# Kernel optimization log

Measured on AMD Instinct MI355X. Metric: run time of the kernel, lower is better.

Reference implementation:

```python
import jax, jax.numpy as jnp
import numpy as np

N, K, W = 500000, 512, 64


def setup_inputs() -> dict:
    key = jax.random.key(0)
    kx, kc = jax.random.split(key)
    X = jax.random.normal(kx, (N, W), dtype=jnp.float32)
    # nn.init.uniform_(codebook.weight, a=-1.0, b=1.0)
    codebook = jax.random.uniform(kc, (K, W), dtype=jnp.float32, minval=-1.0, maxval=1.0)
    return {"X": X, "codebook": codebook}


def reference(X, codebook):
    # torch.cdist (p=2): pairwise Euclidean distances [N, K]
    x2 = jnp.sum(X * X, axis=-1, keepdims=True)          # [N, 1]
    c2 = jnp.sum(codebook * codebook, axis=-1)           # [K]
    d2 = x2 - 2.0 * (X @ codebook.T) + c2[None, :]        # [N, K]
    dist = jnp.sqrt(jnp.maximum(d2, 0.0))
    idx = jnp.argmin(dist, axis=-1)                       # [N] int
    min_dists = jnp.min(dist, axis=-1)                    # [N] == gather(dist, idx)
    return idx, min_dists
```

## Files before the change

kernel.cpp:

```cpp
#include <hip/hip_runtime.h>

#define N_POINTS 500000
#define K_CENT   512
#define W_DIM    64
#define N_JOBS   ((N_POINTS + 63) / 64)
#define SCALE_LO 2048.0f
#define INV_LO   (1.0f / 2048.0f)

typedef _Float16 half8 __attribute__((ext_vector_type(8)));
typedef float    f32x16 __attribute__((ext_vector_type(16)));

__global__ void cvt_kernel(const float* __restrict__ cb,
                           _Float16* __restrict__ cbf) {
    int id = blockIdx.x * 256 + threadIdx.x;
    if (id >= K_CENT * 8) return;
    int c = id >> 3, o = (id & 7) * 8;
    int t = c >> 5, r = c & 31;
    int s = o >> 4, half = (o >> 3) & 1;
    int lane = half * 32 + r;
    const float* src = cb + (size_t)c * W_DIM + o;
    half8 h, l;
#pragma unroll
    for (int j = 0; j < 8; ++j) {
        float w = -2.0f * src[j];
        _Float16 hh = (_Float16)w;
        h[j] = hh;
        l[j] = (_Float16)((w - (float)hh) * SCALE_LO);
    }
    size_t base_h = ((size_t)(t * 2 + 0) * 4 + s) * 512 + (size_t)lane * 8;
    size_t base_l = ((size_t)(t * 2 + 1) * 4 + s) * 512 + (size_t)lane * 8;
    *(half8*)(cbf + base_h) = h;
    *(half8*)(cbf + base_l) = l;
}

__global__ void c2_kernel(const float* __restrict__ cb, float* __restrict__ c2) {
    int c = blockIdx.x * 256 + threadIdx.x;
    if (c >= K_CENT) return;
    const float4* row = (const float4*)(cb + (size_t)c * W_DIM);
    double s = 0.0;
#pragma unroll
    for (int j = 0; j < W_DIM / 4; ++j) {
        float4 v = row[j];
        s += (double)v.x * v.x + (double)v.y * v.y + (double)v.z * v.z + (double)v.w * v.w;
    }
    c2[c] = (float)s;
}

#define CHUNK_BODY(T, CURH, CURL, NXTH, NXTL)                                      \
    {                                                                              \
        int t_ = (T);                                                              \
        if (t_ < 15) {                                                             \
            const _Float16* nb = cbf + (size_t)(t_ + 1) * 4096 + (size_t)lane * 8; \
            NXTH[0] = *(const half8*)(nb + 0 * 512);                               \
            NXTH[1] = *(const half8*)(nb + 1 * 512);                               \
            NXTH[2] = *(const half8*)(nb + 2 * 512);                               \
            NXTH[3] = *(const half8*)(nb + 3 * 512);                               \
            NXTL[0] = *(const half8*)(nb + 2048 + 0 * 512);                        \
            NXTL[1] = *(const half8*)(nb + 2048 + 1 * 512);                        \
            NXTL[2] = *(const half8*)(nb + 2048 + 2 * 512);                        \
            NXTL[3] = *(const half8*)(nb + 2048 + 3 * 512);                        \
        }                                                                          \
        float4 q0 = *(const float4*)&c2s[t_ * 32 + half * 4 + 0];                  \
        float4 q1 = *(const float4*)&c2s[t_ * 32 + half * 4 + 8];                  \
        float4 q2 = *(const float4*)&c2s[t_ * 32 + half * 4 + 16];                 \
        float4 q3 = *(const float4*)&c2s[t_ * 32 + half * 4 + 24];                 \
        f32x16 am0, am1, ac0, ac1;                                                 \
        am0[0]=q0.x; am0[1]=q0.y; am0[2]=q0.z; am0[3]=q0.w;                        \
        am0[4]=q1.x; am0[5]=q1.y; am0[6]=q1.z; am0[7]=q1.w;                        \
        am0[8]=q2.x; am0[9]=q2.y; am0[10]=q2.z; am0[11]=q2.w;                      \
        am0[12]=q3.x; am0[13]=q3.y; am0[14]=q3.z; am0[15]=q3.w;                    \
        am1 = am0;                                                                 \
        _Pragma("unroll")                                                          \
        for (int j = 0; j < 16; ++j) { ac0[j] = 0.f; ac1[j] = 0.f; }               \
        _Pragma("unroll")                                                          \
        for (int s = 0; s < 4; ++s) {                                              \
            am0 = __builtin_amdgcn_mfma_f32_32x32x16_f16(CURH[s], b0h[s], am0, 0, 0, 0); \
            am1 = __builtin_amdgcn_mfma_f32_32x32x16_f16(CURH[s], b1h[s], am1, 0, 0, 0); \
            ac0 = __builtin_amdgcn_mfma_f32_32x32x16_f16(CURL[s], b0h[s], ac0, 0, 0, 0); \
            ac1 = __builtin_amdgcn_mfma_f32_32x32x16_f16(CURL[s], b1h[s], ac1, 0, 0, 0); \
            ac0 = __builtin_amdgcn_mfma_f32_32x32x16_f16(CURH[s], b0l[s], ac0, 0, 0, 0); \
            ac1 = __builtin_amdgcn_mfma_f32_32x32x16_f16(CURH[s], b1l[s], ac1, 0, 0, 0); \
        }                                                                          \
        _Pragma("unroll")                                                          \
        for (int j = 0; j < 16; ++j) {                                             \
            int ci = t_ * 32 + half * 4 + (j >> 2) * 8 + (j & 3);                  \
            float v0 = fmaf(ac0[j], INV_LO, am0[j]);                               \
            if (v0 < bd0) { bd0 = v0; bi0 = ci; }                                  \
            float v1d = fmaf(ac1[j], INV_LO, am1[j]);                              \
            if (v1d < bd1) { bd1 = v1d; bi1 = ci; }                                \
        }                                                                          \
    }

__global__ __launch_bounds__(256, 2)
void kmeans_mfma(const float* __restrict__ X,
                 const _Float16* __restrict__ cbf,
                 const float* __restrict__ c2,
                 float* __restrict__ out_idx,
                 float* __restrict__ out_dist) {
    __shared__ float c2s[K_CENT];
    int tid = threadIdx.x;
    c2s[tid] = c2[tid];
    c2s[tid + 256] = c2[tid + 256];
    __syncthreads();

    int wave = tid >> 6;
    int lane = tid & 63;
    int half = lane >> 5;
    int l31  = lane & 31;
    int kb   = half * 8;

    int job = blockIdx.x * 4 + wave;
    if (job >= N_JOBS) return;

    int  p0 = job * 64 + l31;
    bool v1 = (job * 64 + 32) < N_POINTS;
    int  p1 = v1 ? (p0 + 32) : p0;

    half8 b0h[4], b0l[4], b1h[4], b1l[4];
    float x20 = 0.f, x21 = 0.f;
#pragma unroll
    for (int s = 0; s < 4; ++s) {
        const float4* xa = (const float4*)(X + (size_t)p0 * W_DIM + s * 16 + kb);
        float4 f0 = xa[0], f1 = xa[1];
        float fa[8] = {f0.x, f0.y, f0.z, f0.w, f1.x, f1.y, f1.z, f1.w};
        const float4* xb = (const float4*)(X + (size_t)p1 * W_DIM + s * 16 + kb);
        float4 g0 = xb[0], g1 = xb[1];
        float fb[8] = {g0.x, g0.y, g0.z, g0.w, g1.x, g1.y, g1.z, g1.w};
#pragma unroll
        for (int j = 0; j < 8; ++j) {
            _Float16 h0 = (_Float16)fa[j];
            b0h[s][j] = h0;
            b0l[s][j] = (_Float16)((fa[j] - (float)h0) * SCALE_LO);
            x20 = fmaf(fa[j], fa[j], x20);
            _Float16 h1 = (_Float16)fb[j];
            b1h[s][j] = h1;
            b1l[s][j] = (_Float16)((fb[j] - (float)h1) * SCALE_LO);
            x21 = fmaf(fb[j], fb[j], x21);
        }
    }
    x20 += __shfl_xor(x20, 32);
    x21 += __shfl_xor(x21, 32);

    float bd0 = 3.4e38f, bd1 = 3.4e38f;
    int   bi0 = 0,       bi1 = 0;

    half8 ahA[4], alA[4], ahB[4], alB[4];
    {
        const _Float16* ab = cbf + (size_t)lane * 8;
        ahA[0] = *(const half8*)(ab + 0 * 512);
        ahA[1] = *(const half8*)(ab + 1 * 512);
        ahA[2] = *(const half8*)(ab + 2 * 512);
        ahA[3] = *(const half8*)(ab + 3 * 512);
        alA[0] = *(const half8*)(ab + 2048 + 0 * 512);
        alA[1] = *(const half8*)(ab + 2048 + 1 * 512);
        alA[2] = *(const half8*)(ab + 2048 + 2 * 512);
        alA[3] = *(const half8*)(ab + 2048 + 3 * 512);
    }

#pragma unroll 1
    for (int tt = 0; tt < 8; ++tt) {
        CHUNK_BODY(2 * tt,     ahA, alA, ahB, alB)
        CHUNK_BODY(2 * tt + 1, ahB, alB, ahA, alA)
    }

    {
        float od = __shfl_xor(bd0, 32); int oi = __shfl_xor(bi0, 32);
        if (od < bd0 || (od == bd0 && oi < bi0)) { bd0 = od; bi0 = oi; }
        od = __shfl_xor(bd1, 32); oi = __shfl_xor(bi1, 32);
        if (od < bd1 || (od == bd1 && oi < bi1)) { bd1 = od; bi1 = oi; }
    }

    if (half == 0) {
        out_idx[p0]  = (float)bi0;
        out_dist[p0] = sqrtf(fmaxf(bd0 + x20, 0.f));
        if (v1) {
            out_idx[p1]  = (float)bi1;
            out_dist[p1] = sqrtf(fmaxf(bd1 + x21, 0.f));
        }
    }
}

extern "C" void kernel_launch(void* const* d_in, const int* in_sizes, int n_in,
                              void* d_out, int out_size, void* d_ws, size_t ws_size,
                              hipStream_t stream) {
    const float* X  = (const float*)d_in[0];
    const float* cb = (const float*)d_in[1];
    float* out      = (float*)d_out;

    _Float16* cbf = (_Float16*)d_ws;
    float*    c2  = (float*)(cbf + (size_t)K_CENT * W_DIM * 2);

    hipLaunchKernelGGL(cvt_kernel, dim3((K_CENT * 8 + 255) / 256), dim3(256), 0, stream, cb, cbf);
    hipLaunchKernelGGL(c2_kernel, dim3((K_CENT + 255) / 256), dim3(256), 0, stream, cb, c2);

    hipLaunchKernelGGL(kmeans_mfma, dim3((N_JOBS + 3) / 4), dim3(256), 0, stream,
                       X, cbf, c2, out, out + N_POINTS);
}
```

Measured before the change: 120.8 us.

## Software-pipeline MFMA chunks with argmin and merge hi/lo accumulators

The MFMA work for the next codebook chunk is now issued before the argmin of the previous chunk, using double-buffered accumulators so matrix and vector work can overlap. The main and correction accumulators are merged into one by dropping the 2048 scaling of the low fp16 parts, which removes the extra fma pass. c2 is pre-permuted in shared memory so it loads straight into the accumulator as one vector. Argmin becomes a branchless min-tree with index recovery. Costs: more accumulator registers, and low parts that are no longer scaled may lose fp16 subnormal precision.

Result: faster. 105.2 us (-13.0%).

```diff
diff --git a/kernel.cpp b/kernel.cpp
--- a/kernel.cpp
+++ b/kernel.cpp
@@ -4,8 +4,6 @@
 #define K_CENT   512
 #define W_DIM    64
 #define N_JOBS   ((N_POINTS + 63) / 64)
-#define SCALE_LO 2048.0f
-#define INV_LO   (1.0f / 2048.0f)
 
 typedef _Float16 half8 __attribute__((ext_vector_type(8)));
 typedef float    f32x16 __attribute__((ext_vector_type(16)));
@@ -25,7 +23,7 @@
         float w = -2.0f * src[j];
         _Float16 hh = (_Float16)w;
         h[j] = hh;
-        l[j] = (_Float16)((w - (float)hh) * SCALE_LO);
+        l[j] = (_Float16)(w - (float)hh);
     }
     size_t base_h = ((size_t)(t * 2 + 0) * 4 + s) * 512 + (size_t)lane * 8;
     size_t base_l = ((size_t)(t * 2 + 1) * 4 + s) * 512 + (size_t)lane * 8;
@@ -46,7 +44,7 @@
     c2[c] = (float)s;
 }
 
-#define CHUNK_BODY(T, CURH, CURL, NXTH, NXTL)                                      \
+#define MFMA_CHUNK(T, CURH, CURL, NXTH, NXTL, QC, QN, A0, A1)                      \
     {                                                                              \
         int t_ = (T);                                                              \
         if (t_ < 15) {                                                             \
@@ -59,36 +57,53 @@
             NXTL[1] = *(const half8*)(nb + 2048 + 1 * 512);                        \
             NXTL[2] = *(const half8*)(nb + 2048 + 2 * 512);                        \
             NXTL[3] = *(const half8*)(nb + 2048 + 3 * 512);                        \
+            QN = *(const f32x16*)&c2s[(t_ + 1) * 32 + half16];                     \
         }                                                                          \
-        float4 q0 = *(const float4*)&c2s[t_ * 32 + half * 4 + 0];                  \
-        float4 q1 = *(const float4*)&c2s[t_ * 32 + half * 4 + 8];                  \
-        float4 q2 = *(const float4*)&c2s[t_ * 32 + half * 4 + 16];                 \
-        float4 q3 = *(const float4*)&c2s[t_ * 32 + half * 4 + 24];                 \
-        f32x16 am0, am1, ac0, ac1;                                                 \
-        am0[0]=q0.x; am0[1]=q0.y; am0[2]=q0.z; am0[3]=q0.w;                        \
-        am0[4]=q1.x; am0[5]=q1.y; am0[6]=q1.z; am0[7]=q1.w;                        \
-        am0[8]=q2.x; am0[9]=q2.y; am0[10]=q2.z; am0[11]=q2.w;                      \
-        am0[12]=q3.x; am0[13]=q3.y; am0[14]=q3.z; am0[15]=q3.w;                    \
-        am1 = am0;                                                                 \
+        A0 = __builtin_amdgcn_mfma_f32_32x32x16_f16(CURH[0], b0h[0], QC, 0, 0, 0); \
+        A1 = __builtin_amdgcn_mfma_f32_32x32x16_f16(CURH[0], b1h[0], QC, 0, 0, 0); \
+        A0 = __builtin_amdgcn_mfma_f32_32x32x16_f16(CURL[0], b0h[0], A0, 0, 0, 0); \
+        A1 = __builtin_amdgcn_mfma_f32_32x32x16_f16(CURL[0], b1h[0], A1, 0, 0, 0); \
+        A0 = __builtin_amdgcn_mfma_f32_32x32x16_f16(CURH[0], b0l[0], A0, 0, 0, 0); \
+        A1 = __builtin_amdgcn_mfma_f32_32x32x16_f16(CURH[0], b1l[0], A1, 0, 0, 0); \
         _Pragma("unroll")                                                          \
-        for (int j = 0; j < 16; ++j) { ac0[j] = 0.f; ac1[j] = 0.f; }               \
-        _Pragma("unroll")                                                          \
-        for (int s = 0; s < 4; ++s) {                                              \
-            am0 = __builtin_amdgcn_mfma_f32_32x32x16_f16(CURH[s], b0h[s], am0, 0, 0, 0); \
-            am1 = __builtin_amdgcn_mfma_f32_32x32x16_f16(CURH[s], b1h[s], am1, 0, 0, 0); \
-            ac0 = __builtin_amdgcn_mfma_f32_32x32x16_f16(CURL[s], b0h[s], ac0, 0, 0, 0); \
-            ac1 = __builtin_amdgcn_mfma_f32_32x32x16_f16(CURL[s], b1h[s], ac1, 0, 0, 0); \
-            ac0 = __builtin_amdgcn_mfma_f32_32x32x16_f16(CURH[s], b0l[s], ac0, 0, 0, 0); \
-            ac1 = __builtin_amdgcn_mfma_f32_32x32x16_f16(CURH[s], b1l[s], ac1, 0, 0, 0); \
+        for (int s = 1; s < 4; ++s) {                                              \
+            A0 = __builtin_amdgcn_mfma_f32_32x32x16_f16(CURH[s], b0h[s], A0, 0, 0, 0); \
+            A1 = __builtin_amdgcn_mfma_f32_32x32x16_f16(CURH[s], b1h[s], A1, 0, 0, 0); \
+            A0 = __builtin_amdgcn_mfma_f32_32x32x16_f16(CURL[s], b0h[s], A0, 0, 0, 0); \
+            A1 = __builtin_amdgcn_mfma_f32_32x32x16_f16(CURL[s], b1h[s], A1, 0, 0, 0); \
+            A0 = __builtin_amdgcn_mfma_f32_32x32x16_f16(CURH[s], b0l[s], A0, 0, 0, 0); \
+            A1 = __builtin_amdgcn_mfma_f32_32x32x16_f16(CURH[s], b1l[s], A1, 0, 0, 0); \
         }                                                                          \
-        _Pragma("unroll")                                                          \
-        for (int j = 0; j < 16; ++j) {                                             \
-            int ci = t_ * 32 + half * 4 + (j >> 2) * 8 + (j & 3);                  \
-            float v0 = fmaf(ac0[j], INV_LO, am0[j]);                               \
-            if (v0 < bd0) { bd0 = v0; bi0 = ci; }                                  \
-            float v1d = fmaf(ac1[j], INV_LO, am1[j]);                              \
-            if (v1d < bd1) { bd1 = v1d; bi1 = ci; }                                \
-        }                                                                          \
+    }
+
+#define ARGMIN_TILE(AM, BD, BI, T_)                                            \
+    {                                                                          \
+        float m01 = fminf(AM[0], AM[1]),   m23 = fminf(AM[2], AM[3]);          \
+        float m45 = fminf(AM[4], AM[5]),   m67 = fminf(AM[6], AM[7]);          \
+        float m89 = fminf(AM[8], AM[9]),   mab = fminf(AM[10], AM[11]);        \
+        float mcd = fminf(AM[12], AM[13]), mef = fminf(AM[14], AM[15]);        \
+        float n0 = fminf(m01, m23),  n1 = fminf(m45, m67);                     \
+        float n2 = fminf(m89, mab),  n3 = fminf(mcd, mef);                     \
+        float m  = fminf(fminf(n0, n1), fminf(n2, n3));                        \
+        int ji = 15;                                                           \
+        ji = (AM[14] == m) ? 14 : ji; ji = (AM[13] == m) ? 13 : ji;            \
+        ji = (AM[12] == m) ? 12 : ji; ji = (AM[11] == m) ? 11 : ji;            \
+        ji = (AM[10] == m) ? 10 : ji; ji = (AM[9]  == m) ?  9 : ji;            \
+        ji = (AM[8]  == m) ?  8 : ji; ji = (AM[7]  == m) ?  7 : ji;            \
+        ji = (AM[6]  == m) ?  6 : ji; ji = (AM[5]  == m) ?  5 : ji;            \
+        ji = (AM[4]  == m) ?  4 : ji; ji = (AM[3]  == m) ?  3 : ji;            \
+        ji = (AM[2]  == m) ?  2 : ji; ji = (AM[1]  == m) ?  1 : ji;            \
+        ji = (AM[0]  == m) ?  0 : ji;                                          \
+        int ci = (T_) * 32 + half4 + ((ji >> 2) << 3) + (ji & 3);              \
+        bool imp = m < BD;                                                     \
+        BD = imp ? m : BD;                                                     \
+        BI = imp ? ci : BI;                                                    \
+    }
+
+#define ARGMIN_CHUNK(T, A0, A1)                                                \
+    {                                                                          \
+        ARGMIN_TILE(A0, bd0, bi0, T)                                           \
+        ARGMIN_TILE(A1, bd1, bi1, T)                                           \
     }
 
 __global__ __launch_bounds__(256, 2)
@@ -99,8 +114,14 @@
                  float* __restrict__ out_dist) {
     __shared__ float c2s[K_CENT];
     int tid = threadIdx.x;
-    c2s[tid] = c2[tid];
-    c2s[tid + 256] = c2[tid + 256];
+    {
+        int i = tid;
+        int t = i >> 5, h = (i >> 4) & 1, j = i & 15;
+        c2s[i] = c2[t * 32 + h * 4 + ((j >> 2) << 3) + (j & 3)];
+        i = tid + 256;
+        t = i >> 5; h = (i >> 4) & 1; j = i & 15;
+        c2s[i] = c2[t * 32 + h * 4 + ((j >> 2) << 3) + (j & 3)];
+    }
     __syncthreads();
 
     int wave = tid >> 6;
@@ -108,13 +129,15 @@
     int half = lane >> 5;
     int l31  = lane & 31;
     int kb   = half * 8;
+    int half4  = half * 4;
+    int half16 = half * 16;
 
     int job = blockIdx.x * 4 + wave;
     if (job >= N_JOBS) return;
 
     int  p0 = job * 64 + l31;
-    bool v1 = (job * 64 + 32) < N_POINTS;
-    int  p1 = v1 ? (p0 + 32) : p0;
+    bool v1ok = (job * 64 + 32) < N_POINTS;
+    int  p1 = v1ok ? (p0 + 32) : p0;
 
     half8 b0h[4], b0l[4], b1h[4], b1l[4];
     float x20 = 0.f, x21 = 0.f;
@@ -130,11 +153,11 @@
         for (int j = 0; j < 8; ++j) {
             _Float16 h0 = (_Float16)fa[j];
             b0h[s][j] = h0;
-            b0l[s][j] = (_Float16)((fa[j] - (float)h0) * SCALE_LO);
+            b0l[s][j] = (_Float16)(fa[j] - (float)h0);
             x20 = fmaf(fa[j], fa[j], x20);
             _Float16 h1 = (_Float16)fb[j];
             b1h[s][j] = h1;
-            b1l[s][j] = (_Float16)((fb[j] - (float)h1) * SCALE_LO);
+            b1l[s][j] = (_Float16)(fb[j] - (float)h1);
             x21 = fmaf(fb[j], fb[j], x21);
         }
     }
@@ -145,6 +168,7 @@
     int   bi0 = 0,       bi1 = 0;
 
     half8 ahA[4], alA[4], ahB[4], alB[4];
+    f32x16 qP, qQ, accP0, accP1, accQ0, accQ1;
     {
         const _Float16* ab = cbf + (size_t)lane * 8;
         ahA[0] = *(const half8*)(ab + 0 * 512);
@@ -156,12 +180,20 @@
         alA[2] = *(const half8*)(ab + 2048 + 2 * 512);
         alA[3] = *(const half8*)(ab + 2048 + 3 * 512);
     }
+    qP = *(const f32x16*)&c2s[0 * 32 + half16];
+
+    MFMA_CHUNK(0, ahA, alA, ahB, alB, qP, qQ, accP0, accP1)
 
 #pragma unroll 1
-    for (int tt = 0; tt < 8; ++tt) {
-        CHUNK_BODY(2 * tt,     ahA, alA, ahB, alB)
-        CHUNK_BODY(2 * tt + 1, ahB, alB, ahA, alA)
-    }
+    for (int tt = 0; tt < 7; ++tt) {
+        MFMA_CHUNK(2 * tt + 1, ahB, alB, ahA, alA, qQ, qP, accQ0, accQ1)
+        ARGMIN_CHUNK(2 * tt, accP0, accP1)
+        MFMA_CHUNK(2 * tt + 2, ahA, alA, ahB, alB, qP, qQ, accP0, accP1)
+        ARGMIN_CHUNK(2 * tt + 1, accQ0, accQ1)
+    }
+    MFMA_CHUNK(15, ahB, alB, ahA, alA, qQ, qP, accQ0, accQ1)
+    ARGMIN_CHUNK(14, accP0, accP1)
+    ARGMIN_CHUNK(15, accQ0, accQ1)
 
     {
         float od = __shfl_xor(bd0, 32); int oi = __shfl_xor(bi0, 32);
@@ -173,7 +205,7 @@
     if (half == 0) {
         out_idx[p0]  = (float)bi0;
         out_dist[p0] = sqrtf(fmaxf(bd0 + x20, 0.f));
-        if (v1) {
+        if (v1ok) {
             out_idx[p1]  = (float)bi1;
             out_dist[p1] = sqrtf(fmaxf(bd1 + x21, 0.f));
         }
```
